# Kernel tuning notes

Measured on AMD Instinct MI355X. Metric: run time of the kernel, lower is better.

The kernel has to match this reference:

```python
import jax, jax.numpy as jnp
import numpy as np

N_RAYS = 65536   # 256x256 image
T_SAMPLES = 128  # StratifiedRayStepSampler default
HID = 16         # tiny radiance-field MLP hidden width


def setup_inputs() -> dict:
    key = jax.random.key(0)
    ks = jax.random.split(key, 8)
    o = jax.random.normal(ks[0], (N_RAYS, 3), jnp.float32)
    d = jax.random.normal(ks[1], (N_RAYS, 3), jnp.float32)
    tnear = jnp.zeros((N_RAYS, 1), jnp.float32)
    # tfar in [1,5): guarantees tfar > tnear for every ray
    tfar = 1.0 + 4.0 * jax.random.uniform(ks[2], (N_RAYS, 1), jnp.float32)
    noise = jax.random.uniform(ks[3], (T_SAMPLES, N_RAYS, 1), jnp.float32)
    W1 = jax.random.normal(ks[4], (3, HID), jnp.float32) * 0.5
    b1 = jnp.zeros((HID,), jnp.float32)
    w_sigma = jax.random.normal(ks[5], (HID, 1), jnp.float32) * 0.5
    W_rgb = jax.random.normal(ks[6], (HID, 3), jnp.float32) * 0.5
    return {"o": o, "d": d, "tnear": tnear, "tfar": tfar, "noise": noise,
            "W1": W1, "b1": b1, "w_sigma": w_sigma, "W_rgb": W_rgb}


def reference(o, d, tnear, tfar, noise, W1, b1, w_sigma, W_rgb):
    T = noise.shape[0]
    dnorm = jnp.linalg.norm(d, axis=-1, keepdims=True)            # (N,1)
    # stratified sampling: ts[i] = tnear + (tfar-tnear)*(i+u_i)/T  -> (T,N,1)
    bins = (jnp.arange(T, dtype=o.dtype)[:, None, None] + noise) / T
    ts = tnear[None] + (tfar - tnear)[None] * bins                # (T,N,1)
    # evaluate rays and query radiance field
    xyz = o[None] + ts * d[None]                                  # (T,N,3)
    h = jax.nn.relu(xyz @ W1 + b1)                                # (T,N,HID)
    sigma = jax.nn.softplus(h @ w_sigma)                          # (T,N,1) density
    rgb = jax.nn.sigmoid(h @ W_rgb)                               # (T,N,3) color
    # volumetric integration along sample axis
    delta = jnp.concatenate([ts[1:] - ts[:-1], tfar[None] - ts[-1:]], axis=0)
    sd = sigma * delta * dnorm[None]                              # (T,N,1)
    # exclusive cumsum -> log-transmittance (stable cumprod)
    log_trans = jnp.concatenate(
        [jnp.zeros_like(sd[:1]), -jnp.cumsum(sd[:-1], axis=0)], axis=0)
    weights = jnp.exp(log_trans) * (1.0 - jnp.exp(-sd))           # (T,N,1)
    color = jnp.sum(weights * rgb, axis=0)                        # (N,3)
    depth = jnp.sum(weights * ts, axis=0)                         # (N,1)
    alpha = jnp.sum(weights, axis=0)                              # (N,1)
    return jnp.concatenate([color, depth, alpha], axis=-1)        # (N,5)
```

## Files before the change

### kernel.cpp

```cpp
#include <hip/hip_runtime.h>
#include <math.h>

#define N_RAYS 65536
#define T_SAMPLES 128
#define HID 16
#define HPAIR (HID/2)

#define RAYS_PER_BLOCK 64
#define CHUNKS 4
#define CHUNK_LEN (T_SAMPLES / CHUNKS)
#define PF 4

#define L2E 1.4426950408889634f

typedef float v2f __attribute__((ext_vector_type(2)));

__global__ __launch_bounds__(256, 4) void radiance_kernel(
    const float* __restrict__ o,
    const float* __restrict__ d,
    const float* __restrict__ tnear,
    const float* __restrict__ tfar,
    const float* __restrict__ noise,
    const float* __restrict__ W1,
    const float* __restrict__ b1,
    const float* __restrict__ w_sigma,
    const float* __restrict__ W_rgb,
    float* __restrict__ out)
{
    const int lane  = threadIdx.x & 63;
    const int chunk = threadIdx.x >> 6;
    const int ray   = blockIdx.x * RAYS_PER_BLOCK + lane;

    const int t0 = chunk * CHUNK_LEN;
    const float* __restrict__ nrow = noise + ray;

    const float nz0 = nrow[(size_t)t0 * N_RAYS];
    float nzbuf[PF];
#pragma unroll
    for (int k = 0; k < PF; ++k)
        nzbuf[k] = nrow[(size_t)(t0 + 1 + k) * N_RAYS];

    const float ox = o[ray*3+0], oy = o[ray*3+1], oz = o[ray*3+2];
    const float dx = d[ray*3+0], dy = d[ray*3+1], dz = d[ray*3+2];
    const float tn = tnear[ray];
    const float tf = tfar[ray];
    const float dnorm = sqrtf(dx*dx + dy*dy + dz*dz);
    const float rdn   = 1.0f / dnorm;
    const float sc    = (tf - tn) * (1.0f / (float)T_SAMPLES);

    const float scd = sc * dnorm;
    const float tnd = tn * dnorm;
    const float uf  = tf * dnorm;

    v2f A2[HPAIR], B2[HPAIR];
    v2f WS2[HPAIR], WR2[HPAIR], WG2[HPAIR], WB2[HPAIR];
#pragma unroll
    for (int p = 0; p < HPAIR; ++p) {
#pragma unroll
        for (int h = 0; h < 2; ++h) {
            const int j = 2*p + h;
            const float w0 = W1[0*HID + j], w1 = W1[1*HID + j], w2 = W1[2*HID + j];
            A2[p][h] = fmaf(ox, w0, fmaf(oy, w1, fmaf(oz, w2, b1[j])));
            B2[p][h] = fmaf(dx, w0, fmaf(dy, w1, dz * w2)) * rdn;
            WS2[p][h] = w_sigma[j];
            WR2[p][h] = W_rgb[j*3+0];
            WG2[p][h] = W_rgb[j*3+1];
            WB2[p][h] = W_rgb[j*3+2];
        }
    }

    float u    = fmaf(scd, (float)t0 + nz0, tnd);
    float base = fmaf(scd, (float)(t0 + 1), tnd);

    float lt = 1.0f;
    float cr = 0.f, cg = 0.f, cb = 0.f, cd = 0.f, ca = 0.f;

    for (int ii = 0; ii < CHUNK_LEN; ii += PF) {
#pragma unroll
        for (int k = 0; k < PF; ++k) {
            const int t = t0 + ii + k;

            float u_next = fmaf(scd, nzbuf[k], base);
            if (t == T_SAMPLES - 1) u_next = uf;
            base += scd;

            int rrow = t + 1 + PF;
            if (rrow > T_SAMPLES - 1) rrow = T_SAMPLES - 1;
            nzbuf[k] = nrow[(size_t)rrow * N_RAYS];

            const v2f uu = { u, u };
            v2f sp2 = (v2f)0.f, rr2 = (v2f)0.f, gg2 = (v2f)0.f, bb2 = (v2f)0.f;
#pragma unroll
            for (int p = 0; p < HPAIR; ++p) {
                const v2f h2 = __builtin_elementwise_max(
                    __builtin_elementwise_fma(uu, B2[p], A2[p]), (v2f)0.f);
                sp2 = __builtin_elementwise_fma(h2, WS2[p], sp2);
                rr2 = __builtin_elementwise_fma(h2, WR2[p], rr2);
                gg2 = __builtin_elementwise_fma(h2, WG2[p], gg2);
                bb2 = __builtin_elementwise_fma(h2, WB2[p], bb2);
            }
            const float sp = sp2[0] + sp2[1];
            const float rr = rr2[0] + rr2[1];
            const float gg = gg2[0] + gg2[1];
            const float bb = bb2[0] + bb2[1];

            const float e  = __builtin_amdgcn_exp2f(-fabsf(sp) * L2E);
            const float l2 = fmaf(fmaxf(sp, 0.0f), L2E,
                                  __builtin_amdgcn_logf(1.0f + e));
            const float dd = u_next - u;
            const float et = __builtin_amdgcn_exp2f(-dd * l2);

            const float r = __builtin_amdgcn_rcpf(1.0f + __builtin_amdgcn_exp2f(-rr * L2E));
            const float g = __builtin_amdgcn_rcpf(1.0f + __builtin_amdgcn_exp2f(-gg * L2E));
            const float b = __builtin_amdgcn_rcpf(1.0f + __builtin_amdgcn_exp2f(-bb * L2E));

            const float w = fmaf(-et, lt, lt);
            cr = fmaf(w, r, cr);
            cg = fmaf(w, g, cg);
            cb = fmaf(w, b, cb);
            cd = fmaf(w, u, cd);
            ca += w;
            lt *= et;
            u = u_next;
        }
    }

    __shared__ float s_lt[CHUNKS][RAYS_PER_BLOCK];
    __shared__ float s_acc[CHUNKS][5][RAYS_PER_BLOCK];
    s_lt[chunk][lane] = lt;
    s_acc[chunk][0][lane] = cr;
    s_acc[chunk][1][lane] = cg;
    s_acc[chunk][2][lane] = cb;
    s_acc[chunk][3][lane] = cd;
    s_acc[chunk][4][lane] = ca;
    __syncthreads();

    if (chunk == 0) {
        float scale = 1.0f;
        float a0 = 0.f, a1 = 0.f, a2 = 0.f, a3 = 0.f, a4 = 0.f;
#pragma unroll
        for (int c = 0; c < CHUNKS; ++c) {
            a0 = fmaf(scale, s_acc[c][0][lane], a0);
            a1 = fmaf(scale, s_acc[c][1][lane], a1);
            a2 = fmaf(scale, s_acc[c][2][lane], a2);
            a3 = fmaf(scale, s_acc[c][3][lane], a3);
            a4 = fmaf(scale, s_acc[c][4][lane], a4);
            scale *= s_lt[c][lane];
        }
        out[ray*5+0] = a0;
        out[ray*5+1] = a1;
        out[ray*5+2] = a2;
        out[ray*5+3] = a3 * rdn;
        out[ray*5+4] = a4;
    }
}

extern "C" void kernel_launch(void* const* d_in, const int* in_sizes, int n_in,
                              void* d_out, int out_size, void* d_ws, size_t ws_size,
                              hipStream_t stream) {
    const float* o       = (const float*)d_in[0];
    const float* d       = (const float*)d_in[1];
    const float* tnear   = (const float*)d_in[2];
    const float* tfar    = (const float*)d_in[3];
    const float* noise   = (const float*)d_in[4];
    const float* W1      = (const float*)d_in[5];
    const float* b1      = (const float*)d_in[6];
    const float* w_sigma = (const float*)d_in[7];
    const float* W_rgb   = (const float*)d_in[8];
    float* out = (float*)d_out;

    dim3 block(64 * CHUNKS);
    dim3 grid(N_RAYS / RAYS_PER_BLOCK);
    hipLaunchKernelGGL(radiance_kernel, grid, block, 0, stream,
                       o, d, tnear, tfar, noise, W1, b1, w_sigma, W_rgb, out);
}
```

Before: 112.8 us.

## Split each wave across two sample chunks, simplify softplus, raise occupancy

```diff
diff --git a/kernel.cpp b/kernel.cpp
--- a/kernel.cpp
+++ b/kernel.cpp
@@ -6,8 +6,8 @@
 #define HID 16
 #define HPAIR (HID/2)
 
-#define RAYS_PER_BLOCK 64
-#define CHUNKS 4
+#define RAYS_PER_BLOCK 32
+#define CHUNKS 8
 #define CHUNK_LEN (T_SAMPLES / CHUNKS)
 #define PF 4
 
@@ -15,7 +15,7 @@
 
 typedef float v2f __attribute__((ext_vector_type(2)));
 
-__global__ __launch_bounds__(256, 4) void radiance_kernel(
+__global__ __launch_bounds__(256, 6) void radiance_kernel(
     const float* __restrict__ o,
     const float* __restrict__ d,
     const float* __restrict__ tnear,
@@ -27,9 +27,12 @@
     const float* __restrict__ W_rgb,
     float* __restrict__ out)
 {
-    const int lane  = threadIdx.x & 63;
-    const int chunk = threadIdx.x >> 6;
-    const int ray   = blockIdx.x * RAYS_PER_BLOCK + lane;
+    const int tid   = threadIdx.x;
+    const int wv    = tid >> 6;
+    const int lane  = tid & 63;
+    const int rlane = lane & 31;
+    const int chunk = wv * 2 + (lane >> 5);
+    const int ray   = blockIdx.x * RAYS_PER_BLOCK + rlane;
 
     const int t0 = chunk * CHUNK_LEN;
     const float* __restrict__ nrow = noise + ray;
@@ -69,8 +72,14 @@
         }
     }
 
+    asm volatile("" : "+v"(A2[0]), "+v"(A2[1]), "+v"(A2[2]), "+v"(A2[3]),
+                      "+v"(A2[4]), "+v"(A2[5]), "+v"(A2[6]), "+v"(A2[7]),
+                      "+v"(B2[0]), "+v"(B2[1]), "+v"(B2[2]), "+v"(B2[3]),
+                      "+v"(B2[4]), "+v"(B2[5]), "+v"(B2[6]), "+v"(B2[7]));
+
     float u    = fmaf(scd, (float)t0 + nz0, tnd);
     float base = fmaf(scd, (float)(t0 + 1), tnd);
+    const bool lastchunk = (chunk == CHUNKS - 1);
 
     float lt = 1.0f;
     float cr = 0.f, cg = 0.f, cb = 0.f, cd = 0.f, ca = 0.f;
@@ -81,7 +90,8 @@
             const int t = t0 + ii + k;
 
             float u_next = fmaf(scd, nzbuf[k], base);
-            if (t == T_SAMPLES - 1) u_next = uf;
+            if (ii + k == CHUNK_LEN - 1)
+                u_next = lastchunk ? uf : u_next;
             base += scd;
 
             int rrow = t + 1 + PF;
@@ -104,9 +114,8 @@
             const float gg = gg2[0] + gg2[1];
             const float bb = bb2[0] + bb2[1];
 
-            const float e  = __builtin_amdgcn_exp2f(-fabsf(sp) * L2E);
-            const float l2 = fmaf(fmaxf(sp, 0.0f), L2E,
-                                  __builtin_amdgcn_logf(1.0f + e));
+            const float l2 = __builtin_amdgcn_logf(
+                1.0f + __builtin_amdgcn_exp2f(sp * L2E));
             const float dd = u_next - u;
             const float et = __builtin_amdgcn_exp2f(-dd * l2);
 
@@ -127,12 +136,12 @@
 
     __shared__ float s_lt[CHUNKS][RAYS_PER_BLOCK];
     __shared__ float s_acc[CHUNKS][5][RAYS_PER_BLOCK];
-    s_lt[chunk][lane] = lt;
-    s_acc[chunk][0][lane] = cr;
-    s_acc[chunk][1][lane] = cg;
-    s_acc[chunk][2][lane] = cb;
-    s_acc[chunk][3][lane] = cd;
-    s_acc[chunk][4][lane] = ca;
+    s_lt[chunk][rlane] = lt;
+    s_acc[chunk][0][rlane] = cr;
+    s_acc[chunk][1][rlane] = cg;
+    s_acc[chunk][2][rlane] = cb;
+    s_acc[chunk][3][rlane] = cd;
+    s_acc[chunk][4][rlane] = ca;
     __syncthreads();
 
     if (chunk == 0) {
@@ -140,12 +149,12 @@
         float a0 = 0.f, a1 = 0.f, a2 = 0.f, a3 = 0.f, a4 = 0.f;
 #pragma unroll
         for (int c = 0; c < CHUNKS; ++c) {
-            a0 = fmaf(scale, s_acc[c][0][lane], a0);
-            a1 = fmaf(scale, s_acc[c][1][lane], a1);
-            a2 = fmaf(scale, s_acc[c][2][lane], a2);
-            a3 = fmaf(scale, s_acc[c][3][lane], a3);
-            a4 = fmaf(scale, s_acc[c][4][lane], a4);
-            scale *= s_lt[c][lane];
+            a0 = fmaf(scale, s_acc[c][0][rlane], a0);
+            a1 = fmaf(scale, s_acc[c][1][rlane], a1);
+            a2 = fmaf(scale, s_acc[c][2][rlane], a2);
+            a3 = fmaf(scale, s_acc[c][3][rlane], a3);
+            a4 = fmaf(scale, s_acc[c][4][rlane], a4);
+            scale *= s_lt[c][rlane];
         }
         out[ray*5+0] = a0;
         out[ray*5+1] = a1;
@@ -169,7 +178,7 @@
     const float* W_rgb   = (const float*)d_in[8];
     float* out = (float*)d_out;
 
-    dim3 block(64 * CHUNKS);
+    dim3 block(256);
     dim3 grid(N_RAYS / RAYS_PER_BLOCK);
     hipLaunchKernelGGL(radiance_kernel, grid, block, 0, stream,
                        o, d, tnear, tfar, noise, W1, b1, w_sigma, W_rgb, out);
```

New measurement: 113.4 us. No clear change (+0.6%).
